# Optimization experiments

Measured on AMD Instinct MI355X. Metric: run time of the kernel, lower is better.

## Reference

```python
import jax, jax.numpy as jnp
import numpy as np


def setup_inputs() -> dict:
    key = jax.random.key(0)
    B, S, L = 64, 64, 8192
    history = jax.random.uniform(key, (B, S, L), dtype=jnp.float32)
    return {"history": history, "topk": 30}


def reference(history, topk):
    # top@k branch of repeatPast:
    # cumulative label counts over admissions, then keep only the top-k
    # most frequent labels per (batch, step) and multiply by their counts.
    whole_history = jnp.cumsum(history, axis=1)            # [B, S, L]
    # argsort descending over labels (matches torch.argsort(..., descending=True))
    order = jnp.argsort(-whole_history, axis=2)            # [B, S, L]
    # rank[i,j,l] = position of label l in the descending order
    rank = jnp.argsort(order, axis=2)                      # [B, S, L]
    mask = (rank < topk).astype(whole_history.dtype)       # scatter-1 at top-k indices
    return mask * whole_history
```

## Files before the change

kernel.cpp:

```cpp
#include <hip/hip_runtime.h>


constexpr int B_ = 64, S_ = 64, L_ = 8192;
constexpr int THREADS = 256;
constexpr int VPT = L_ / THREADS;
constexpr int CHUNK = 4;
constexpr int NCHUNK = S_ / CHUNK;
constexpr int CAND_MAX = 160;

__device__ const float ZTAB[16] = {
    0.0f, 1.70f, 2.14f, 2.27f, 2.32f, 2.34f, 2.35f, 2.36f,
    2.37f, 2.375f, 2.38f, 2.385f, 2.39f, 2.39f, 2.395f, 2.395f};

__global__ __launch_bounds__(THREADS)
void cumsum_boundaries(const float* __restrict__ in, float* __restrict__ out)
{
    int t = blockIdx.x * THREADS + threadIdx.x;
    int b = t >> 13;
    int l = t & (L_ - 1);
    const float* p = in + ((size_t)b << 19) + l;
    float* o = out + ((size_t)b << 19) + l;
    float acc = 0.f;
#pragma unroll
    for (int s = 0; s < S_; ++s) {
        acc += p[(size_t)s << 13];
        if ((s & 3) == 3 && s != S_ - 1)
            o[(size_t)(s + 1) << 13] = acc;
    }
}

__global__ __launch_bounds__(THREADS)
void select_topk(const float* __restrict__ in, const int* __restrict__ topk_p,
                 float* __restrict__ out)
{
    __shared__ int wtot[4];
    __shared__ unsigned candv[CAND_MAX];
    __shared__ unsigned short candi[CAND_MAX];
    __shared__ int s_cnt;
    __shared__ unsigned s_Tb;
    __shared__ int s_aux;

    const int tid = threadIdx.x;
    const int lane = tid & 63;
    const int wv = tid >> 6;
    const int blk = blockIdx.x;
    const int b = blk >> 4;
    const int c = blk & (NCHUNK - 1);
    const int s0 = c * CHUNK;
    const int k = *topk_p;

    const float* base = in + ((size_t)b * S_ + s0) * L_ + tid * VPT;
    float* obase = out + ((size_t)b * S_ + s0) * L_ + tid * VPT;

    float acc[VPT];
    if (c == 0) {
#pragma unroll
        for (int j = 0; j < VPT; ++j) acc[j] = 0.f;
    } else {
        const float4* ep = (const float4*)obase;
#pragma unroll
        for (int q = 0; q < VPT / 4; ++q) {
            float4 v = ep[q];
            acc[4*q+0] = v.x; acc[4*q+1] = v.y; acc[4*q+2] = v.z; acc[4*q+3] = v.w;
        }
    }

    for (int r = 0; r < CHUNK; ++r) {
        const int s = s0 + r;
        {
            const float4* rp = (const float4*)(base + (size_t)r * L_);
#pragma unroll
            for (int q = 0; q < VPT / 4; ++q) {
                float4 v = rp[q];
                acc[4*q+0] += v.x; acc[4*q+1] += v.y; acc[4*q+2] += v.z; acc[4*q+3] += v.w;
            }
        }

        const int n = s + 1;
        const float mu = 0.5f * (float)n;
        const float sig = sqrtf((float)n * (1.0f / 12.0f));
        const float z = (n < 16) ? ZTAB[n] : 2.40f;

        unsigned lo = 0u;
        unsigned hi = __float_as_uint((float)n);
        int hiC = 0;
        unsigned T = __float_as_uint(mu + z * sig);
        if (!(T > lo && T < hi)) T = lo + ((hi - lo) >> 1);

        unsigned Tsel = 0;
        int path = 0;
        int needEq = 0;

        for (int it = 0; it < 40; ++it) {
            int cnt = 0;
#pragma unroll
            for (int j = 0; j < VPT; ++j)
                cnt += (__float_as_uint(acc[j]) >= T) ? 1 : 0;
#pragma unroll
            for (int off = 32; off >= 1; off >>= 1) cnt += __shfl_xor(cnt, off, 64);
            __syncthreads();
            if (lane == 0) wtot[wv] = cnt;
            __syncthreads();
            const int ctot = wtot[0] + wtot[1] + wtot[2] + wtot[3];

            if (ctot >= k && ctot <= CAND_MAX) { Tsel = T; path = 0; break; }
            if (ctot >= k) { lo = T; } else { hi = T; hiC = ctot; }
            if (hi - lo <= 1u) { Tsel = lo; path = 1; needEq = k - hiC; break; }
            T = lo + ((hi - lo) >> 1);
        }

        unsigned Tb;
        int idxT = 0, excl = 0;

        if (path == 0) {
            if (tid == 0) s_cnt = 0;
            __syncthreads();
#pragma unroll
            for (int j = 0; j < VPT; ++j) {
                unsigned u = __float_as_uint(acc[j]);
                if (u >= Tsel) {
                    int p = atomicAdd(&s_cnt, 1);
                    if (p < CAND_MAX) {
                        candv[p] = u;
                        candi[p] = (unsigned short)(tid * VPT + j);
                    }
                }
            }
            __syncthreads();
            const int cc = s_cnt;
            if (tid < cc) {
                unsigned mv = candv[tid];
                int mi = candi[tid];
                int rk = 0;
                for (int j2 = 0; j2 < cc; ++j2) {
                    unsigned ov = candv[j2];
                    int oi = candi[j2];
                    rk += ((ov > mv) || (ov == mv && oi < mi)) ? 1 : 0;
                }
                if (rk == k - 1) { s_Tb = mv; s_aux = mi; }
            }
            __syncthreads();
            Tb = s_Tb;
            idxT = s_aux;
        } else {
            int myeq = 0;
#pragma unroll
            for (int j = 0; j < VPT; ++j)
                myeq += (__float_as_uint(acc[j]) == Tsel) ? 1 : 0;
            int sc = myeq;
#pragma unroll
            for (int off = 1; off < 64; off <<= 1) {
                int o = __shfl_up(sc, off, 64);
                if (lane >= off) sc += o;
            }
            __syncthreads();
            if (lane == 63) wtot[wv] = sc;
            __syncthreads();
            excl = sc - myeq;
            for (int w2 = 0; w2 < wv; ++w2) excl += wtot[w2];
            Tb = Tsel;
        }

        float4* ow = (float4*)(obase + (size_t)r * L_);
        int run = excl;
#pragma unroll
        for (int q = 0; q < VPT / 4; ++q) {
            float res[4];
#pragma unroll
            for (int m = 0; m < 4; ++m) {
                const int j = 4 * q + m;
                const unsigned u = __float_as_uint(acc[j]);
                bool inc;
                if (path == 0) {
                    inc = (u > Tb) || (u == Tb && (tid * VPT + j) <= idxT);
                } else {
                    if (u > Tb) inc = true;
                    else if (u == Tb) { inc = (run < needEq); ++run; }
                    else inc = false;
                }
                res[m] = inc ? acc[j] : 0.f;
            }
            float4 o4; o4.x = res[0]; o4.y = res[1]; o4.z = res[2]; o4.w = res[3];
            ow[q] = o4;
        }
    }
}

extern "C" void kernel_launch(void* const* d_in, const int* in_sizes, int n_in,
                              void* d_out, int out_size, void* d_ws, size_t ws_size,
                              hipStream_t stream) {
    const float* hist_in = (const float*)d_in[0];
    const int* topk = (const int*)d_in[1];
    float* out = (float*)d_out;

    hipLaunchKernelGGL(cumsum_boundaries, dim3((B_ * L_) / THREADS), dim3(THREADS),
                       0, stream, hist_in, out);
    hipLaunchKernelGGL(select_topk, dim3(B_ * NCHUNK), dim3(THREADS),
                       0, stream, hist_in, topk, out);
}
```

Baseline: 104.3 us.

## Materialize full cumsum and select top-k with one block per row

The cumsum kernel now writes every prefix row instead of only chunk boundaries, and the selection kernel launches one block per (batch, step) row that reads the precomputed cumsum in place. This removes the serial four-row loop per block and quadruples the number of independent blocks, exposing more parallelism for the latency-bound threshold bisection. The cost is extra global memory traffic, since the full cumsum is written once and read back. A barrier is also merged by resetting the candidate counter inside the first bisection iteration.

```diff
diff --git a/kernel.cpp b/kernel.cpp
--- a/kernel.cpp
+++ b/kernel.cpp
@@ -4,8 +4,6 @@
 constexpr int B_ = 64, S_ = 64, L_ = 8192;
 constexpr int THREADS = 256;
 constexpr int VPT = L_ / THREADS;
-constexpr int CHUNK = 4;
-constexpr int NCHUNK = S_ / CHUNK;
 constexpr int CAND_MAX = 160;
 
 __device__ const float ZTAB[16] = {
@@ -13,7 +11,7 @@
     2.37f, 2.375f, 2.38f, 2.385f, 2.39f, 2.39f, 2.395f, 2.395f};
 
 __global__ __launch_bounds__(THREADS)
-void cumsum_boundaries(const float* __restrict__ in, float* __restrict__ out)
+void cumsum_full(const float* __restrict__ in, float* __restrict__ out)
 {
     int t = blockIdx.x * THREADS + threadIdx.x;
     int b = t >> 13;
@@ -24,14 +22,12 @@
 #pragma unroll
     for (int s = 0; s < S_; ++s) {
         acc += p[(size_t)s << 13];
-        if ((s & 3) == 3 && s != S_ - 1)
-            o[(size_t)(s + 1) << 13] = acc;
+        o[(size_t)s << 13] = acc;
     }
 }
 
 __global__ __launch_bounds__(THREADS)
-void select_topk(const float* __restrict__ in, const int* __restrict__ topk_p,
-                 float* __restrict__ out)
+void select_row(const int* __restrict__ topk_p, float* __restrict__ out)
 {
     __shared__ int wtot[4];
     __shared__ unsigned candv[CAND_MAX];
@@ -44,145 +40,126 @@
     const int lane = tid & 63;
     const int wv = tid >> 6;
     const int blk = blockIdx.x;
-    const int b = blk >> 4;
-    const int c = blk & (NCHUNK - 1);
-    const int s0 = c * CHUNK;
+    const int s = blk & (S_ - 1);
     const int k = *topk_p;
 
-    const float* base = in + ((size_t)b * S_ + s0) * L_ + tid * VPT;
-    float* obase = out + ((size_t)b * S_ + s0) * L_ + tid * VPT;
+    float* row = out + (size_t)blk * L_ + tid * VPT;
 
     float acc[VPT];
-    if (c == 0) {
-#pragma unroll
-        for (int j = 0; j < VPT; ++j) acc[j] = 0.f;
-    } else {
-        const float4* ep = (const float4*)obase;
+    {
+        const float4* rp = (const float4*)row;
 #pragma unroll
         for (int q = 0; q < VPT / 4; ++q) {
-            float4 v = ep[q];
+            float4 v = rp[q];
             acc[4*q+0] = v.x; acc[4*q+1] = v.y; acc[4*q+2] = v.z; acc[4*q+3] = v.w;
         }
     }
 
-    for (int r = 0; r < CHUNK; ++r) {
-        const int s = s0 + r;
-        {
-            const float4* rp = (const float4*)(base + (size_t)r * L_);
+    const int n = s + 1;
+    const float mu = 0.5f * (float)n;
+    const float sig = sqrtf((float)n * (1.0f / 12.0f));
+    const float z = (n < 16) ? ZTAB[n] : 2.40f;
+
+    unsigned lo = 0u;
+    unsigned hi = __float_as_uint((float)n);
+    int hiC = 0;
+    unsigned T = __float_as_uint(mu + z * sig);
+    if (!(T > lo && T < hi)) T = lo + ((hi - lo) >> 1);
+
+    unsigned Tsel = 0;
+    int path = 0;
+    int needEq = 0;
+
+    for (int it = 0; it < 40; ++it) {
+        int cnt = 0;
 #pragma unroll
-            for (int q = 0; q < VPT / 4; ++q) {
-                float4 v = rp[q];
-                acc[4*q+0] += v.x; acc[4*q+1] += v.y; acc[4*q+2] += v.z; acc[4*q+3] += v.w;
+        for (int j = 0; j < VPT; ++j)
+            cnt += (__float_as_uint(acc[j]) >= T) ? 1 : 0;
+#pragma unroll
+        for (int off = 32; off >= 1; off >>= 1) cnt += __shfl_xor(cnt, off, 64);
+        if (it != 0) __syncthreads();
+        if (lane == 0) wtot[wv] = cnt;
+        if (tid == 0) s_cnt = 0;
+        __syncthreads();
+        const int ctot = wtot[0] + wtot[1] + wtot[2] + wtot[3];
+
+        if (ctot >= k && ctot <= CAND_MAX) { Tsel = T; path = 0; break; }
+        if (ctot >= k) { lo = T; } else { hi = T; hiC = ctot; }
+        if (hi - lo <= 1u) { Tsel = lo; path = 1; needEq = k - hiC; break; }
+        T = lo + ((hi - lo) >> 1);
+    }
+
+    unsigned Tb;
+    int idxT = 0, excl = 0;
+
+    if (path == 0) {
+#pragma unroll
+        for (int j = 0; j < VPT; ++j) {
+            unsigned u = __float_as_uint(acc[j]);
+            if (u >= Tsel) {
+                int p = atomicAdd(&s_cnt, 1);
+                if (p < CAND_MAX) {
+                    candv[p] = u;
+                    candi[p] = (unsigned short)(tid * VPT + j);
+                }
             }
         }
+        __syncthreads();
+        const int cc = s_cnt;
+        if (tid < cc) {
+            unsigned mv = candv[tid];
+            int mi = candi[tid];
+            int rk = 0;
+            for (int j2 = 0; j2 < cc; ++j2) {
+                unsigned ov = candv[j2];
+                int oi = candi[j2];
+                rk += ((ov > mv) || (ov == mv && oi < mi)) ? 1 : 0;
+            }
+            if (rk == k - 1) { s_Tb = mv; s_aux = mi; }
+        }
+        __syncthreads();
+        Tb = s_Tb;
+        idxT = s_aux;
+    } else {
+        int myeq = 0;
+#pragma unroll
+        for (int j = 0; j < VPT; ++j)
+            myeq += (__float_as_uint(acc[j]) == Tsel) ? 1 : 0;
+        int sc = myeq;
+#pragma unroll
+        for (int off = 1; off < 64; off <<= 1) {
+            int o = __shfl_up(sc, off, 64);
+            if (lane >= off) sc += o;
+        }
+        __syncthreads();
+        if (lane == 63) wtot[wv] = sc;
+        __syncthreads();
+        excl = sc - myeq;
+        for (int w2 = 0; w2 < wv; ++w2) excl += wtot[w2];
+        Tb = Tsel;
+    }
 
-        const int n = s + 1;
-        const float mu = 0.5f * (float)n;
-        const float sig = sqrtf((float)n * (1.0f / 12.0f));
-        const float z = (n < 16) ? ZTAB[n] : 2.40f;
-
-        unsigned lo = 0u;
-        unsigned hi = __float_as_uint((float)n);
-        int hiC = 0;
-        unsigned T = __float_as_uint(mu + z * sig);
-        if (!(T > lo && T < hi)) T = lo + ((hi - lo) >> 1);
-
-        unsigned Tsel = 0;
-        int path = 0;
-        int needEq = 0;
-
-        for (int it = 0; it < 40; ++it) {
-            int cnt = 0;
+    float4* ow = (float4*)row;
+    int run = excl;
 #pragma unroll
-            for (int j = 0; j < VPT; ++j)
-                cnt += (__float_as_uint(acc[j]) >= T) ? 1 : 0;
+    for (int q = 0; q < VPT / 4; ++q) {
+        float res[4];
 #pragma unroll
-            for (int off = 32; off >= 1; off >>= 1) cnt += __shfl_xor(cnt, off, 64);
-            __syncthreads();
-            if (lane == 0) wtot[wv] = cnt;
-            __syncthreads();
-            const int ctot = wtot[0] + wtot[1] + wtot[2] + wtot[3];
-
-            if (ctot >= k && ctot <= CAND_MAX) { Tsel = T; path = 0; break; }
-            if (ctot >= k) { lo = T; } else { hi = T; hiC = ctot; }
-            if (hi - lo <= 1u) { Tsel = lo; path = 1; needEq = k - hiC; break; }
-            T = lo + ((hi - lo) >> 1);
+        for (int m = 0; m < 4; ++m) {
+            const int j = 4 * q + m;
+            const unsigned u = __float_as_uint(acc[j]);
+            bool inc;
+            if (path == 0) {
+                inc = (u > Tb) || (u == Tb && (tid * VPT + j) <= idxT);
+            } else {
+                if (u > Tb) inc = true;
+                else if (u == Tb) { inc = (run < needEq); ++run; }
+                else inc = false;
+            }
+            res[m] = inc ? acc[j] : 0.f;
         }
-
-        unsigned Tb;
-        int idxT = 0, excl = 0;
-
-        if (path == 0) {
-            if (tid == 0) s_cnt = 0;
-            __syncthreads();
-#pragma unroll
-            for (int j = 0; j < VPT; ++j) {
-                unsigned u = __float_as_uint(acc[j]);
-                if (u >= Tsel) {
-                    int p = atomicAdd(&s_cnt, 1);
-                    if (p < CAND_MAX) {
-                        candv[p] = u;
-                        candi[p] = (unsigned short)(tid * VPT + j);
-                    }
-                }
-            }
-            __syncthreads();
-            const int cc = s_cnt;
-            if (tid < cc) {
-                unsigned mv = candv[tid];
-                int mi = candi[tid];
-                int rk = 0;
-                for (int j2 = 0; j2 < cc; ++j2) {
-                    unsigned ov = candv[j2];
-                    int oi = candi[j2];
-                    rk += ((ov > mv) || (ov == mv && oi < mi)) ? 1 : 0;
-                }
-                if (rk == k - 1) { s_Tb = mv; s_aux = mi; }
-            }
-            __syncthreads();
-            Tb = s_Tb;
-            idxT = s_aux;
-        } else {
-            int myeq = 0;
-#pragma unroll
-            for (int j = 0; j < VPT; ++j)
-                myeq += (__float_as_uint(acc[j]) == Tsel) ? 1 : 0;
-            int sc = myeq;
-#pragma unroll
-            for (int off = 1; off < 64; off <<= 1) {
-                int o = __shfl_up(sc, off, 64);
-                if (lane >= off) sc += o;
-            }
-            __syncthreads();
-            if (lane == 63) wtot[wv] = sc;
-            __syncthreads();
-            excl = sc - myeq;
-            for (int w2 = 0; w2 < wv; ++w2) excl += wtot[w2];
-            Tb = Tsel;
-        }
-
-        float4* ow = (float4*)(obase + (size_t)r * L_);
-        int run = excl;
-#pragma unroll
-        for (int q = 0; q < VPT / 4; ++q) {
-            float res[4];
-#pragma unroll
-            for (int m = 0; m < 4; ++m) {
-                const int j = 4 * q + m;
-                const unsigned u = __float_as_uint(acc[j]);
-                bool inc;
-                if (path == 0) {
-                    inc = (u > Tb) || (u == Tb && (tid * VPT + j) <= idxT);
-                } else {
-                    if (u > Tb) inc = true;
-                    else if (u == Tb) { inc = (run < needEq); ++run; }
-                    else inc = false;
-                }
-                res[m] = inc ? acc[j] : 0.f;
-            }
-            float4 o4; o4.x = res[0]; o4.y = res[1]; o4.z = res[2]; o4.w = res[3];
-            ow[q] = o4;
-        }
+        float4 o4; o4.x = res[0]; o4.y = res[1]; o4.z = res[2]; o4.w = res[3];
+        ow[q] = o4;
     }
 }
 
@@ -193,8 +170,8 @@
     const int* topk = (const int*)d_in[1];
     float* out = (float*)d_out;
 
-    hipLaunchKernelGGL(cumsum_boundaries, dim3((B_ * L_) / THREADS), dim3(THREADS),
+    hipLaunchKernelGGL(cumsum_full, dim3((B_ * L_) / THREADS), dim3(THREADS),
                        0, stream, hist_in, out);
-    hipLaunchKernelGGL(select_topk, dim3(B_ * NCHUNK), dim3(THREADS),
-                       0, stream, hist_in, topk, out);
+    hipLaunchKernelGGL(select_row, dim3(B_ * S_), dim3(THREADS),
+                       0, stream, topk, out);
 }
```

Measured after the change: 109.1 us. +4.5%, slower.
